# Optimization experiments

Measured on AMD Instinct MI355X. Metric: run time of the kernel, lower is better.

Reference implementation:

```python
import jax, jax.numpy as jnp
import numpy as np

N_NODES = 100000
N_EDGES = 1600000
IN_F, HID_F, OUT_F = 48, 16, 60


def _graph_conv(x, src, dst, W_rel, b_rel, W_root):
    # PyG GraphConv (aggr='add'): out = lin_rel(sum_{j in N(i)} x_j) + lin_root(x_i)
    agg = jax.ops.segment_sum(x[src], dst, num_segments=N_NODES)  # [N, F_in]
    return agg @ W_rel + b_rel + x @ W_root


def setup_inputs() -> dict:
    key = jax.random.key(0)
    ks = jax.random.split(key, 9)
    glorot = lambda k, fi, fo: jax.random.normal(k, (fi, fo), jnp.float32) * np.sqrt(2.0 / (fi + fo))
    x = jax.random.normal(ks[0], (N_NODES, IN_F), jnp.float32)
    edge_index = jax.random.randint(ks[1], (2, N_EDGES), 0, N_NODES, dtype=jnp.int64)
    return {
        "x": x,
        "edge_index": edge_index,
        "W1_rel": glorot(ks[2], IN_F, HID_F),
        "b1": jnp.zeros((HID_F,), jnp.float32),
        "W1_root": glorot(ks[3], IN_F, HID_F),
        "W1b_rel": glorot(ks[4], HID_F, HID_F),
        "b1b": jnp.zeros((HID_F,), jnp.float32),
        "W1b_root": glorot(ks[5], HID_F, HID_F),
        "W2_rel": glorot(ks[6], HID_F, OUT_F),
        "b2": jnp.zeros((OUT_F,), jnp.float32),
        "W2_root": glorot(ks[7], HID_F, OUT_F),
    }


def reference(x, edge_index, W1_rel, b1, W1_root, W1b_rel, b1b, W1b_root, W2_rel, b2, W2_root):
    src, dst = edge_index[0], edge_index[1]
    h = jnp.tanh(_graph_conv(x, src, dst, W1_rel, b1, W1_root))
    h = jnp.tanh(_graph_conv(h, src, dst, W1b_rel, b1b, W1b_root))
    # F.dropout(training=self.training): identity in eval mode
    out = _graph_conv(h, src, dst, W2_rel, b2, W2_root)  # [N, OUT_F]
    return out
```

## Files before the change

### kernel.cpp

```cpp
#include <hip/hip_runtime.h>
#include <hip/hip_bf16.h>
#include <cmath>

#define N_NODES 100000
#define N_EDGES 1600000
#define IN_F 48
#define HID_F 16
#define OUT_F 60

#define BKT 256
#define NBKT ((N_NODES + BKT - 1) / BKT)
#define EPB 8192
#define NB_P ((N_EDGES + EPB - 1) / EPB)
#define EPB_H 2048
#define NB_H ((N_EDGES + EPB_H - 1) / EPB_H)

typedef __hip_bfloat16 bf16;
typedef float f32x4 __attribute__((ext_vector_type(4)));

__device__ __forceinline__ float bf2f(unsigned short u)
{
    return __uint_as_float(((unsigned int)u) << 16);
}

__global__ __launch_bounds__(256) void k_bhist(
    const int* __restrict__ dst, int* __restrict__ bcnt)
{
    __shared__ int h[NBKT];
    for (int i = threadIdx.x; i < NBKT; i += 256) h[i] = 0;
    __syncthreads();
    int base = blockIdx.x * EPB_H;
    #pragma unroll
    for (int i = 0; i < EPB_H / 256; ++i) {
        int e = base + i * 256 + threadIdx.x;
        if (e < N_EDGES) atomicAdd(&h[dst[e] >> 8], 1);
    }
    __syncthreads();
    for (int i = threadIdx.x; i < NBKT; i += 256)
        if (h[i]) atomicAdd(&bcnt[i], h[i]);
}

__global__ __launch_bounds__(1024) void k_bscan(
    const int* __restrict__ bcnt, int* __restrict__ base, int* __restrict__ cursor)
{
    __shared__ int tmp[1024];
    int v = (threadIdx.x < NBKT) ? bcnt[threadIdx.x] : 0;
    tmp[threadIdx.x] = v;
    __syncthreads();
    #pragma unroll
    for (int ofs = 1; ofs < 1024; ofs <<= 1) {
        int a = (threadIdx.x >= ofs) ? tmp[threadIdx.x - ofs] : 0;
        __syncthreads();
        tmp[threadIdx.x] += a;
        __syncthreads();
    }
    if (threadIdx.x < NBKT) {
        int ex = tmp[threadIdx.x] - v;
        base[threadIdx.x] = ex;
        cursor[threadIdx.x] = ex;
    }
    if (threadIdx.x == 0) base[NBKT] = N_EDGES;
}

__global__ __launch_bounds__(1024) void k_partition(
    const int* __restrict__ src, const int* __restrict__ dst,
    int* __restrict__ cursor, unsigned int* __restrict__ pk)
{
    __shared__ int cnt[NBKT];
    __shared__ int bb[NBKT];
    for (int i = threadIdx.x; i < NBKT; i += 1024) cnt[i] = 0;
    __syncthreads();
    int e0 = blockIdx.x * EPB;
    int dloc[EPB / 1024];
    #pragma unroll
    for (int i = 0; i < EPB / 1024; ++i) {
        int e = e0 + i * 1024 + threadIdx.x;
        dloc[i] = (e < N_EDGES) ? dst[e] : -1;
        if (dloc[i] >= 0) atomicAdd(&cnt[dloc[i] >> 8], 1);
    }
    __syncthreads();
    for (int i = threadIdx.x; i < NBKT; i += 1024) {
        int c = cnt[i];
        bb[i] = c ? atomicAdd(&cursor[i], c) : 0;
        cnt[i] = 0;
    }
    __syncthreads();
    #pragma unroll
    for (int i = 0; i < EPB / 1024; ++i) {
        int e = e0 + i * 1024 + threadIdx.x;
        int d = dloc[i];
        if (d >= 0) {
            int b = d >> 8;
            int r = atomicAdd(&cnt[b], 1);
            pk[bb[b] + r] = ((unsigned int)src[e] << 8) | (unsigned int)(d & 255);
        }
    }
}

__global__ __launch_bounds__(1024) void k_bucket_csr(
    const int* __restrict__ base, const unsigned int* __restrict__ pk,
    int* __restrict__ off_end, int* __restrict__ csr)
{
    __shared__ int hist[BKT];
    __shared__ int tmp[BKT];
    __shared__ int cur[BKT];
    int b = blockIdx.x;
    int e0 = base[b], e1 = base[b + 1];
    if (threadIdx.x < BKT) hist[threadIdx.x] = 0;
    __syncthreads();
    for (int e = e0 + threadIdx.x; e < e1; e += 1024)
        atomicAdd(&hist[pk[e] & 255u], 1);
    __syncthreads();
    int v = 0;
    if (threadIdx.x < BKT) { v = hist[threadIdx.x]; tmp[threadIdx.x] = v; }
    __syncthreads();
    #pragma unroll
    for (int ofs = 1; ofs < BKT; ofs <<= 1) {
        int a = (threadIdx.x < BKT && threadIdx.x >= ofs) ? tmp[threadIdx.x - ofs] : 0;
        __syncthreads();
        if (threadIdx.x < BKT) tmp[threadIdx.x] += a;
        __syncthreads();
    }
    if (threadIdx.x < BKT) {
        int incl = tmp[threadIdx.x];
        cur[threadIdx.x] = e0 + incl - v;
        int n = b * BKT + threadIdx.x;
        if (n < N_NODES) off_end[n] = e0 + incl;
    }
    __syncthreads();
    for (int e = e0 + threadIdx.x; e < e1; e += 1024) {
        unsigned int p = pk[e];
        int pos = atomicAdd(&cur[p & 255u], 1);
        csr[pos] = (int)(p >> 8);
    }
}

__device__ __forceinline__ float gather_feat(
    const int* __restrict__ off_end, const int* __restrict__ csr_src,
    const unsigned short* __restrict__ Yu, int n, int lane)
{
    int e0 = (n == 0) ? 0 : off_end[n - 1];
    int e1 = off_end[n];
    float a0 = 0.f, a1 = 0.f, a2 = 0.f, a3 = 0.f;
    int e = e0;
    for (; e + 3 < e1; e += 4) {
        int s0 = csr_src[e];
        int s1 = csr_src[e + 1];
        int s2 = csr_src[e + 2];
        int s3 = csr_src[e + 3];
        a0 += bf2f(Yu[(size_t)s0 * HID_F + lane]);
        a1 += bf2f(Yu[(size_t)s1 * HID_F + lane]);
        a2 += bf2f(Yu[(size_t)s2 * HID_F + lane]);
        a3 += bf2f(Yu[(size_t)s3 * HID_F + lane]);
    }
    for (; e < e1; ++e)
        a0 += bf2f(Yu[(size_t)csr_src[e] * HID_F + lane]);
    return (a0 + a1) + (a2 + a3);
}

__global__ __launch_bounds__(256) void k1_lin48(
    const float* __restrict__ x, const float* __restrict__ Wrel,
    const float* __restrict__ b, const float* __restrict__ Wroot,
    bf16* __restrict__ Ya, float* __restrict__ R, int* __restrict__ bcnt)
{
    if (blockIdx.x == 0) {
        for (int i = threadIdx.x; i < NBKT; i += 256) bcnt[i] = 0;
    }

    __shared__ float sWrel[IN_F * HID_F];
    __shared__ float sWroot[IN_F * HID_F];
    __shared__ float sb[HID_F];
    for (int i = threadIdx.x; i < IN_F * HID_F; i += 256) {
        sWrel[i]  = Wrel[i];
        sWroot[i] = Wroot[i];
    }
    if (threadIdx.x < HID_F) sb[threadIdx.x] = b[threadIdx.x];
    __syncthreads();

    int n = blockIdx.x * 256 + threadIdx.x;
    if (n >= N_NODES) return;

    float xv[IN_F];
    const f32x4* xr = reinterpret_cast<const f32x4*>(x + (size_t)n * IN_F);
    #pragma unroll
    for (int i = 0; i < IN_F / 4; ++i) {
        f32x4 t = __builtin_nontemporal_load(xr + i);
        xv[4*i+0] = t.x; xv[4*i+1] = t.y; xv[4*i+2] = t.z; xv[4*i+3] = t.w;
    }

    float accR[HID_F], accT[HID_F];
    #pragma unroll
    for (int f = 0; f < HID_F; ++f) { accR[f] = 0.0f; accT[f] = sb[f]; }

    #pragma unroll 6
    for (int k = 0; k < IN_F; ++k) {
        float xk = xv[k];
        #pragma unroll
        for (int f = 0; f < HID_F; ++f) {
            accR[f] = fmaf(xk, sWrel[k*HID_F + f], accR[f]);
            accT[f] = fmaf(xk, sWroot[k*HID_F + f], accT[f]);
        }
    }

    union { bf16 h[HID_F]; uint4 q[2]; } yo;
    #pragma unroll
    for (int f = 0; f < HID_F; ++f) yo.h[f] = __float2bfloat16(accR[f]);
    uint4* yq = reinterpret_cast<uint4*>(Ya + (size_t)n * HID_F);
    yq[0] = yo.q[0]; yq[1] = yo.q[1];

    float4* rr = reinterpret_cast<float4*>(R + (size_t)n * HID_F);
    #pragma unroll
    for (int q = 0; q < HID_F / 4; ++q)
        rr[q] = make_float4(accT[4*q], accT[4*q+1], accT[4*q+2], accT[4*q+3]);
}

__global__ __launch_bounds__(256) void kA_gather_lin16(
    const int* __restrict__ off_end, const int* __restrict__ csr_src,
    const bf16* __restrict__ Ya, float* __restrict__ R,
    const float* __restrict__ Wrel, const float* __restrict__ bb,
    const float* __restrict__ Wroot, bf16* __restrict__ Yb)
{
    __shared__ float sWrel[HID_F * HID_F];
    __shared__ float sWroot[HID_F * HID_F];
    __shared__ float sb[HID_F];
    if (threadIdx.x < HID_F * HID_F) {
        sWrel[threadIdx.x]  = Wrel[threadIdx.x];
        sWroot[threadIdx.x] = Wroot[threadIdx.x];
    }
    if (threadIdx.x < HID_F) sb[threadIdx.x] = bb[threadIdx.x];
    __syncthreads();

    int t = blockIdx.x * 256 + threadIdx.x;
    int n = t >> 4;
    int lane = t & 15;
    if (n >= N_NODES) return;

    float agg = gather_feat(off_end, csr_src,
                            (const unsigned short*)Ya, n, lane);
    float h = tanhf(R[(size_t)n * HID_F + lane] + agg);

    int base = threadIdx.x & 48;
    float accR = 0.f, accT = sb[lane];
    #pragma unroll
    for (int k = 0; k < HID_F; ++k) {
        float hk = __shfl(h, base | k);
        accR = fmaf(hk, sWrel[k * HID_F + lane], accR);
        accT = fmaf(hk, sWroot[k * HID_F + lane], accT);
    }

    ((unsigned short*)Yb)[(size_t)n * HID_F + lane] =
        (unsigned short)(__bfloat16_as_ushort(__float2bfloat16(accR)));
    R[(size_t)n * HID_F + lane] = accT;
}

__global__ __launch_bounds__(256) void kB_gather_tanh(
    const int* __restrict__ off_end, const int* __restrict__ csr_src,
    const bf16* __restrict__ Yb, const float* __restrict__ R,
    bf16* __restrict__ Ya)
{
    int t = blockIdx.x * 256 + threadIdx.x;
    int n = t >> 4;
    int lane = t & 15;
    if (n >= N_NODES) return;

    float agg = gather_feat(off_end, csr_src,
                            (const unsigned short*)Yb, n, lane);
    float h2 = tanhf(R[(size_t)n * HID_F + lane] + agg);
    ((unsigned short*)Ya)[(size_t)n * HID_F + lane] =
        (unsigned short)(__bfloat16_as_ushort(__float2bfloat16(h2)));
}

__global__ __launch_bounds__(256) void kC_gather_out(
    const int* __restrict__ off_end, const int* __restrict__ csr_src,
    const bf16* __restrict__ Ya,
    const float* __restrict__ Wrel, const float* __restrict__ b2,
    const float* __restrict__ Wroot, float* __restrict__ out)
{
    __shared__ float sWrel[HID_F * OUT_F];
    __shared__ float sWroot[HID_F * OUT_F];
    __shared__ float sb[OUT_F];
    for (int i = threadIdx.x; i < HID_F * OUT_F; i += 256) {
        sWrel[i]  = Wrel[i];
        sWroot[i] = Wroot[i];
    }
    if (threadIdx.x < OUT_F) sb[threadIdx.x] = b2[threadIdx.x];
    __syncthreads();

    int t = blockIdx.x * 256 + threadIdx.x;
    int n = t >> 4;
    int lane = t & 15;
    if (n >= N_NODES) return;

    float agg = gather_feat(off_end, csr_src,
                            (const unsigned short*)Ya, n, lane);
    float h2 = bf2f(((const unsigned short*)Ya)[(size_t)n * HID_F + lane]);

    int base = threadIdx.x & 48;
    float acc[4];
    #pragma unroll
    for (int q = 0; q < 4; ++q) {
        int j = q * 16 + lane;
        acc[q] = (j < OUT_F) ? sb[j] : 0.f;
    }
    #pragma unroll
    for (int k = 0; k < HID_F; ++k) {
        float ak = __shfl(agg, base | k);
        float hk = __shfl(h2,  base | k);
        #pragma unroll
        for (int q = 0; q < 4; ++q) {
            int j = q * 16 + lane;
            if (j < OUT_F) {
                acc[q] = fmaf(ak, sWrel[k * OUT_F + j], acc[q]);
                acc[q] = fmaf(hk, sWroot[k * OUT_F + j], acc[q]);
            }
        }
    }
    float* orow = out + (size_t)n * OUT_F;
    #pragma unroll
    for (int q = 0; q < 4; ++q) {
        int j = q * 16 + lane;
        if (j < OUT_F) __builtin_nontemporal_store(acc[q], orow + j);
    }
}

extern "C" void kernel_launch(void* const* d_in, const int* in_sizes, int n_in,
                              void* d_out, int out_size, void* d_ws, size_t ws_size,
                              hipStream_t stream)
{
    const float* x        = (const float*)d_in[0];
    const int*   ei       = (const int*)d_in[1];
    const float* W1_rel   = (const float*)d_in[2];
    const float* b1       = (const float*)d_in[3];
    const float* W1_root  = (const float*)d_in[4];
    const float* W1b_rel  = (const float*)d_in[5];
    const float* b1b      = (const float*)d_in[6];
    const float* W1b_root = (const float*)d_in[7];
    const float* W2_rel   = (const float*)d_in[8];
    const float* b2       = (const float*)d_in[9];
    const float* W2_root  = (const float*)d_in[10];
    float* out = (float*)d_out;

    const int* src = ei;
    const int* dst = ei + N_EDGES;

    bf16* Ya     = (bf16*)d_ws;
    bf16* Yb     = Ya + (size_t)N_NODES * HID_F;
    float* R     = (float*)(Yb + (size_t)N_NODES * HID_F);
    int* csr     = (int*)(R + (size_t)N_NODES * HID_F);
    int* off_end = csr + N_EDGES;
    int* bcnt    = off_end + N_NODES;
    int* base    = bcnt + NBKT;
    int* cursor  = base + NBKT + 1;
    unsigned int* pk = (unsigned int*)d_out;

    const int nb_n = (N_NODES + 255) / 256;
    const int nb_g = (N_NODES * HID_F + 255) / 256;

    k1_lin48<<<nb_n, 256, 0, stream>>>(x, W1_rel, b1, W1_root, Ya, R, bcnt);

    k_bhist<<<NB_H, 256, 0, stream>>>(dst, bcnt);
    k_bscan<<<1, 1024, 0, stream>>>(bcnt, base, cursor);
    k_partition<<<NB_P, 1024, 0, stream>>>(src, dst, cursor, pk);
    k_bucket_csr<<<NBKT, 1024, 0, stream>>>(base, pk, off_end, csr);

    kA_gather_lin16<<<nb_g, 256, 0, stream>>>(off_end, csr, Ya, R,
                                              W1b_rel, b1b, W1b_root, Yb);
    kB_gather_tanh<<<nb_g, 256, 0, stream>>>(off_end, csr, Yb, R, Ya);
    kC_gather_out<<<nb_g, 256, 0, stream>>>(off_end, csr, Ya,
                                            W2_rel, b2, W2_root, out);
}
```

Measured before the change: 176.3 us.

## Use two threads per node with 16-byte vector gathers in GNN aggregation

Changes the three gather kernels from 16 threads per node (one bf16 feature each) to 2 threads per node, each loading 8 bf16 features as a uint4. The neighbour features are read with wide 16-byte loads and the dense layer outputs are written vectorised. This cuts the number of load instructions and redundant index loads per edge by 8x. In exchange each thread holds more registers (kC keeps 30 accumulators), and launching 8x fewer threads reduces parallelism for hiding gather latency.

Result: slower. 193.7 us (+9.8%).

```diff
diff --git a/kernel.cpp b/kernel.cpp
--- a/kernel.cpp
+++ b/kernel.cpp
@@ -17,10 +17,17 @@
 
 typedef __hip_bfloat16 bf16;
 typedef float f32x4 __attribute__((ext_vector_type(4)));
-
-__device__ __forceinline__ float bf2f(unsigned short u)
-{
-    return __uint_as_float(((unsigned int)u) << 16);
+typedef unsigned int u32;
+
+__device__ __forceinline__ float bf2f(u32 u)
+{
+    return __uint_as_float(u << 16);
+}
+__device__ __forceinline__ u32 pack_bf2(float lo, float hi)
+{
+    u32 l = __bfloat16_as_ushort(__float2bfloat16(lo));
+    u32 h = __bfloat16_as_ushort(__float2bfloat16(hi));
+    return l | (h << 16);
 }
 
 __global__ __launch_bounds__(256) void k_bhist(
@@ -64,7 +71,7 @@
 
 __global__ __launch_bounds__(1024) void k_partition(
     const int* __restrict__ src, const int* __restrict__ dst,
-    int* __restrict__ cursor, unsigned int* __restrict__ pk)
+    int* __restrict__ cursor, u32* __restrict__ pk)
 {
     __shared__ int cnt[NBKT];
     __shared__ int bb[NBKT];
@@ -92,13 +99,13 @@
         if (d >= 0) {
             int b = d >> 8;
             int r = atomicAdd(&cnt[b], 1);
-            pk[bb[b] + r] = ((unsigned int)src[e] << 8) | (unsigned int)(d & 255);
+            pk[bb[b] + r] = ((u32)src[e] << 8) | (u32)(d & 255);
         }
     }
 }
 
 __global__ __launch_bounds__(1024) void k_bucket_csr(
-    const int* __restrict__ base, const unsigned int* __restrict__ pk,
+    const int* __restrict__ base, const u32* __restrict__ pk,
     int* __restrict__ off_end, int* __restrict__ csr)
 {
     __shared__ int hist[BKT];
@@ -129,33 +136,56 @@
     }
     __syncthreads();
     for (int e = e0 + threadIdx.x; e < e1; e += 1024) {
-        unsigned int p = pk[e];
+        u32 p = pk[e];
         int pos = atomicAdd(&cur[p & 255u], 1);
         csr[pos] = (int)(p >> 8);
     }
 }
 
-__device__ __forceinline__ float gather_feat(
+__device__ __forceinline__ void gather8(
     const int* __restrict__ off_end, const int* __restrict__ csr_src,
-    const unsigned short* __restrict__ Yu, int n, int lane)
+    const uint4* __restrict__ Yu, int n, int lane, float* __restrict__ outp)
 {
     int e0 = (n == 0) ? 0 : off_end[n - 1];
     int e1 = off_end[n];
-    float a0 = 0.f, a1 = 0.f, a2 = 0.f, a3 = 0.f;
+    float a[8] = {0.f,0.f,0.f,0.f,0.f,0.f,0.f,0.f};
+    float b[8] = {0.f,0.f,0.f,0.f,0.f,0.f,0.f,0.f};
     int e = e0;
     for (; e + 3 < e1; e += 4) {
         int s0 = csr_src[e];
         int s1 = csr_src[e + 1];
         int s2 = csr_src[e + 2];
         int s3 = csr_src[e + 3];
-        a0 += bf2f(Yu[(size_t)s0 * HID_F + lane]);
-        a1 += bf2f(Yu[(size_t)s1 * HID_F + lane]);
-        a2 += bf2f(Yu[(size_t)s2 * HID_F + lane]);
-        a3 += bf2f(Yu[(size_t)s3 * HID_F + lane]);
-    }
-    for (; e < e1; ++e)
-        a0 += bf2f(Yu[(size_t)csr_src[e] * HID_F + lane]);
-    return (a0 + a1) + (a2 + a3);
+        uint4 u0 = Yu[(size_t)s0 * 2 + lane];
+        uint4 u1 = Yu[(size_t)s1 * 2 + lane];
+        uint4 u2 = Yu[(size_t)s2 * 2 + lane];
+        uint4 u3 = Yu[(size_t)s3 * 2 + lane];
+        a[0] += bf2f(u0.x & 0xffffu); a[1] += bf2f(u0.x >> 16);
+        a[2] += bf2f(u0.y & 0xffffu); a[3] += bf2f(u0.y >> 16);
+        a[4] += bf2f(u0.z & 0xffffu); a[5] += bf2f(u0.z >> 16);
+        a[6] += bf2f(u0.w & 0xffffu); a[7] += bf2f(u0.w >> 16);
+        b[0] += bf2f(u1.x & 0xffffu); b[1] += bf2f(u1.x >> 16);
+        b[2] += bf2f(u1.y & 0xffffu); b[3] += bf2f(u1.y >> 16);
+        b[4] += bf2f(u1.z & 0xffffu); b[5] += bf2f(u1.z >> 16);
+        b[6] += bf2f(u1.w & 0xffffu); b[7] += bf2f(u1.w >> 16);
+        a[0] += bf2f(u2.x & 0xffffu); a[1] += bf2f(u2.x >> 16);
+        a[2] += bf2f(u2.y & 0xffffu); a[3] += bf2f(u2.y >> 16);
+        a[4] += bf2f(u2.z & 0xffffu); a[5] += bf2f(u2.z >> 16);
+        a[6] += bf2f(u2.w & 0xffffu); a[7] += bf2f(u2.w >> 16);
+        b[0] += bf2f(u3.x & 0xffffu); b[1] += bf2f(u3.x >> 16);
+        b[2] += bf2f(u3.y & 0xffffu); b[3] += bf2f(u3.y >> 16);
+        b[4] += bf2f(u3.z & 0xffffu); b[5] += bf2f(u3.z >> 16);
+        b[6] += bf2f(u3.w & 0xffffu); b[7] += bf2f(u3.w >> 16);
+    }
+    for (; e < e1; ++e) {
+        uint4 u = Yu[(size_t)csr_src[e] * 2 + lane];
+        a[0] += bf2f(u.x & 0xffffu); a[1] += bf2f(u.x >> 16);
+        a[2] += bf2f(u.y & 0xffffu); a[3] += bf2f(u.y >> 16);
+        a[4] += bf2f(u.z & 0xffffu); a[5] += bf2f(u.z >> 16);
+        a[6] += bf2f(u.w & 0xffffu); a[7] += bf2f(u.w >> 16);
+    }
+    #pragma unroll
+    for (int i = 0; i < 8; ++i) outp[i] = a[i] + b[i];
 }
 
 __global__ __launch_bounds__(256) void k1_lin48(
@@ -231,26 +261,47 @@
     __syncthreads();
 
     int t = blockIdx.x * 256 + threadIdx.x;
-    int n = t >> 4;
-    int lane = t & 15;
+    int n = t >> 1;
+    int lane = t & 1;
     if (n >= N_NODES) return;
 
-    float agg = gather_feat(off_end, csr_src,
-                            (const unsigned short*)Ya, n, lane);
-    float h = tanhf(R[(size_t)n * HID_F + lane] + agg);
-
-    int base = threadIdx.x & 48;
-    float accR = 0.f, accT = sb[lane];
+    float agg[8];
+    gather8(off_end, csr_src, (const uint4*)Ya, n, lane, agg);
+
+    const float4* rrow = reinterpret_cast<const float4*>(R + (size_t)n * HID_F) + lane * 2;
+    float4 r0 = rrow[0], r1 = rrow[1];
+    float h[8];
+    h[0] = tanhf(r0.x + agg[0]); h[1] = tanhf(r0.y + agg[1]);
+    h[2] = tanhf(r0.z + agg[2]); h[3] = tanhf(r0.w + agg[3]);
+    h[4] = tanhf(r1.x + agg[4]); h[5] = tanhf(r1.y + agg[5]);
+    h[6] = tanhf(r1.z + agg[6]); h[7] = tanhf(r1.w + agg[7]);
+
+    int base = threadIdx.x & 62;
+    int fbase = lane * 8;
+    float accR[8], accT[8];
+    #pragma unroll
+    for (int j = 0; j < 8; ++j) { accR[j] = 0.f; accT[j] = sb[fbase + j]; }
+
     #pragma unroll
     for (int k = 0; k < HID_F; ++k) {
-        float hk = __shfl(h, base | k);
-        accR = fmaf(hk, sWrel[k * HID_F + lane], accR);
-        accT = fmaf(hk, sWroot[k * HID_F + lane], accT);
-    }
-
-    ((unsigned short*)Yb)[(size_t)n * HID_F + lane] =
-        (unsigned short)(__bfloat16_as_ushort(__float2bfloat16(accR)));
-    R[(size_t)n * HID_F + lane] = accT;
+        float hk = __shfl(h[k & 7], base + (k >> 3));
+        #pragma unroll
+        for (int j = 0; j < 8; ++j) {
+            accR[j] = fmaf(hk, sWrel[k * HID_F + fbase + j], accR[j]);
+            accT[j] = fmaf(hk, sWroot[k * HID_F + fbase + j], accT[j]);
+        }
+    }
+
+    uint4 yo;
+    yo.x = pack_bf2(accR[0], accR[1]);
+    yo.y = pack_bf2(accR[2], accR[3]);
+    yo.z = pack_bf2(accR[4], accR[5]);
+    yo.w = pack_bf2(accR[6], accR[7]);
+    ((uint4*)Yb)[(size_t)n * 2 + lane] = yo;
+
+    float4* rw = reinterpret_cast<float4*>(R + (size_t)n * HID_F) + lane * 2;
+    rw[0] = make_float4(accT[0], accT[1], accT[2], accT[3]);
+    rw[1] = make_float4(accT[4], accT[5], accT[6], accT[7]);
 }
 
 __global__ __launch_bounds__(256) void kB_gather_tanh(
@@ -259,15 +310,20 @@
     bf16* __restrict__ Ya)
 {
     int t = blockIdx.x * 256 + threadIdx.x;
-    int n = t >> 4;
-    int lane = t & 15;
+    int n = t >> 1;
+    int lane = t & 1;
     if (n >= N_NODES) return;
 
-    float agg = gather_feat(off_end, csr_src,
-                            (const unsigned short*)Yb, n, lane);
-    float h2 = tanhf(R[(size_t)n * HID_F + lane] + agg);
-    ((unsigned short*)Ya)[(size_t)n * HID_F + lane] =
-        (unsigned short)(__bfloat16_as_ushort(__float2bfloat16(h2)));
+    float agg[8];
+    gather8(off_end, csr_src, (const uint4*)Yb, n, lane, agg);
+    const float4* rrow = reinterpret_cast<const float4*>(R + (size_t)n * HID_F) + lane * 2;
+    float4 r0 = rrow[0], r1 = rrow[1];
+    uint4 yo;
+    yo.x = pack_bf2(tanhf(r0.x + agg[0]), tanhf(r0.y + agg[1]));
+    yo.y = pack_bf2(tanhf(r0.z + agg[2]), tanhf(r0.w + agg[3]));
+    yo.z = pack_bf2(tanhf(r1.x + agg[4]), tanhf(r1.y + agg[5]));
+    yo.w = pack_bf2(tanhf(r1.z + agg[6]), tanhf(r1.w + agg[7]));
+    ((uint4*)Ya)[(size_t)n * 2 + lane] = yo;
 }
 
 __global__ __launch_bounds__(256) void kC_gather_out(
@@ -287,40 +343,40 @@
     __syncthreads();
 
     int t = blockIdx.x * 256 + threadIdx.x;
-    int n = t >> 4;
-    int lane = t & 15;
+    int n = t >> 1;
+    int lane = t & 1;
     if (n >= N_NODES) return;
 
-    float agg = gather_feat(off_end, csr_src,
-                            (const unsigned short*)Ya, n, lane);
-    float h2 = bf2f(((const unsigned short*)Ya)[(size_t)n * HID_F + lane]);
-
-    int base = threadIdx.x & 48;
-    float acc[4];
-    #pragma unroll
-    for (int q = 0; q < 4; ++q) {
-        int j = q * 16 + lane;
-        acc[q] = (j < OUT_F) ? sb[j] : 0.f;
-    }
+    float agg[8];
+    gather8(off_end, csr_src, (const uint4*)Ya, n, lane, agg);
+    uint4 hown = ((const uint4*)Ya)[(size_t)n * 2 + lane];
+    float h[8];
+    h[0] = bf2f(hown.x & 0xffffu); h[1] = bf2f(hown.x >> 16);
+    h[2] = bf2f(hown.y & 0xffffu); h[3] = bf2f(hown.y >> 16);
+    h[4] = bf2f(hown.z & 0xffffu); h[5] = bf2f(hown.z >> 16);
+    h[6] = bf2f(hown.w & 0xffffu); h[7] = bf2f(hown.w >> 16);
+
+    int base = threadIdx.x & 62;
+    float acc[30];
+    #pragma unroll
+    for (int q = 0; q < 30; ++q) acc[q] = sb[q * 2 + lane];
+
     #pragma unroll
     for (int k = 0; k < HID_F; ++k) {
-        float ak = __shfl(agg, base | k);
-        float hk = __shfl(h2,  base | k);
+        float av = __shfl(agg[k & 7], base + (k >> 3));
+        float gv = __shfl(h[k & 7],   base + (k >> 3));
+        const float* wr = sWrel  + k * OUT_F + lane;
+        const float* wt = sWroot + k * OUT_F + lane;
         #pragma unroll
-        for (int q = 0; q < 4; ++q) {
-            int j = q * 16 + lane;
-            if (j < OUT_F) {
-                acc[q] = fmaf(ak, sWrel[k * OUT_F + j], acc[q]);
-                acc[q] = fmaf(hk, sWroot[k * OUT_F + j], acc[q]);
-            }
+        for (int q = 0; q < 30; ++q) {
+            acc[q] = fmaf(av, wr[q * 2], acc[q]);
+            acc[q] = fmaf(gv, wt[q * 2], acc[q]);
         }
     }
-    float* orow = out + (size_t)n * OUT_F;
-    #pragma unroll
-    for (int q = 0; q < 4; ++q) {
-        int j = q * 16 + lane;
-        if (j < OUT_F) __builtin_nontemporal_store(acc[q], orow + j);
-    }
+    float* orow = out + (size_t)n * OUT_F + lane;
+    #pragma unroll
+    for (int q = 0; q < 30; ++q)
+        __builtin_nontemporal_store(acc[q], orow + q * 2);
 }
 
 extern "C" void kernel_launch(void* const* d_in, const int* in_sizes, int n_in,
@@ -351,10 +407,10 @@
     int* bcnt    = off_end + N_NODES;
     int* base    = bcnt + NBKT;
     int* cursor  = base + NBKT + 1;
-    unsigned int* pk = (unsigned int*)d_out;
-
-    const int nb_n = (N_NODES + 255) / 256;
-    const int nb_g = (N_NODES * HID_F + 255) / 256;
+    u32* pk      = (u32*)d_out;
+
+    const int nb_n  = (N_NODES + 255) / 256;
+    const int nb_g2 = (N_NODES * 2 + 255) / 256;
 
     k1_lin48<<<nb_n, 256, 0, stream>>>(x, W1_rel, b1, W1_root, Ya, R, bcnt);
 
@@ -363,9 +419,9 @@
     k_partition<<<NB_P, 1024, 0, stream>>>(src, dst, cursor, pk);
     k_bucket_csr<<<NBKT, 1024, 0, stream>>>(base, pk, off_end, csr);
 
-    kA_gather_lin16<<<nb_g, 256, 0, stream>>>(off_end, csr, Ya, R,
-                                              W1b_rel, b1b, W1b_root, Yb);
-    kB_gather_tanh<<<nb_g, 256, 0, stream>>>(off_end, csr, Yb, R, Ya);
-    kC_gather_out<<<nb_g, 256, 0, stream>>>(off_end, csr, Ya,
-                                            W2_rel, b2, W2_root, out);
-}
+    kA_gather_lin16<<<nb_g2, 256, 0, stream>>>(off_end, csr, Ya, R,
+                                               W1b_rel, b1b, W1b_root, Yb);
+    kB_gather_tanh<<<nb_g2, 256, 0, stream>>>(off_end, csr, Yb, R, Ya);
+    kC_gather_out<<<nb_g2, 256, 0, stream>>>(off_end, csr, Ya,
+                                             W2_rel, b2, W2_root, out);
+}
```
